# Optimization experiments

Measured on AMD Instinct MI355X. Metric: run time of the kernel, lower is better.

The kernel has to match this reference:

```python
import jax, jax.numpy as jnp
import numpy as np

BLOCK_SIZE = 64
NEG_INF = -10000.0


def setup_inputs() -> dict:
    key = jax.random.key(0)
    k1, k2, k3 = jax.random.split(key, 3)
    bs, h, s, d = 4, 12, 4096, 64
    Q = jax.random.normal(k1, (bs, h, s, d), dtype=jnp.float32)
    K = jax.random.normal(k2, (bs, h, s, d), dtype=jnp.float32)
    V = jax.random.normal(k3, (bs, h, s, d), dtype=jnp.float32)
    mask = jnp.ones((bs, s), dtype=jnp.float32)
    return {"Q": Q, "K": K, "V": V, "mask": mask}


def reference(Q, K, V, mask):
    bs, h, orig_len, d = Q.shape
    bsz = BLOCK_SIZE
    num_block = (orig_len + bsz - 1) // bsz
    pad_len = num_block * bsz - orig_len
    if pad_len > 0:
        pad4 = ((0, 0), (0, 0), (0, pad_len), (0, 0))
        Q = jnp.pad(Q, pad4)
        K = jnp.pad(K, pad4)
        V = jnp.pad(V, pad4)
        mask = jnp.pad(mask, ((0, 0), (0, pad_len)))
    # reshape into non-overlapping blocks: [bs, h, nb, bsz, d]
    Qb = Q.reshape(bs, h, num_block, bsz, d)
    Kb = K.reshape(bs, h, num_block, bsz, d)
    Vb = V.reshape(bs, h, num_block, bsz, d)
    # block-local scores (no 1/sqrt(d) scaling in the original): [bs,h,nb,bsz,bsz]
    scores = jnp.einsum('bhnxd,bhnyd->bhnxy', Qb, Kb)
    # key-side additive mask per block: -10000 where mask == 0
    remove = (mask == 0.0).reshape(bs, 1, num_block, 1, bsz)  # on key axis y
    scores = scores + jnp.where(remove, jnp.float32(NEG_INF), jnp.float32(0.0))
    probs = jax.nn.softmax(scores, axis=-1)
    # zero out rows whose query position is masked
    q_removed = (mask == 0.0).reshape(bs, 1, num_block, bsz, 1)
    probs = jnp.where(q_removed, jnp.float32(0.0), probs)
    out = jnp.einsum('bhnxy,bhnyd->bhnxd', probs, Vb)
    out = out.reshape(bs, h, num_block * bsz, d)[:, :, :orig_len, :]
    return out
```

## Files before the change

kernel.cpp:

```cpp
#include <hip/hip_runtime.h>


typedef __attribute__((ext_vector_type(8))) short bf16x8;
typedef __attribute__((ext_vector_type(4))) float f32x4;
typedef __attribute__((ext_vector_type(4))) unsigned short us4;

#define MFMA16(a, b, c) __builtin_amdgcn_mfma_f32_16x16x32_bf16((a), (b), (c), 0, 0, 0)
#define SWZ(byteoff, row) ((byteoff) ^ (((row) & 7) << 4))

static __device__ __forceinline__ unsigned short f2bf(float x) {
    union { float f; unsigned int u; } v; v.f = x;
    unsigned int r = v.u + 0x7fffu + ((v.u >> 16) & 1u);
    return (unsigned short)(r >> 16);
}
static __device__ __forceinline__ float bf2f(unsigned short b) {
    union { float f; unsigned int u; } v; v.u = ((unsigned int)b) << 16;
    return v.f;
}

__global__ __launch_bounds__(256) void lsa_kernel(
    const float* __restrict__ Q, const float* __restrict__ K,
    const float* __restrict__ V, const float* __restrict__ M,
    float* __restrict__ O)
{
    __shared__ unsigned short Kh[4096];
    __shared__ unsigned short Kl[4096];
    __shared__ unsigned short VT[4096];
    __shared__ float maskv[64];

    const int tid = threadIdx.x;
    const int gid = blockIdx.x;
    const size_t base = (size_t)gid * 4096;

    const int lane = tid & 63;
    const int wv   = tid >> 6;
    const int cc   = lane & 15;
    const int gg   = lane >> 4;
    const int qrow = wv * 16 + cc;

    const float4* Kg = (const float4*)(K + base);
    const float4* Vg = (const float4*)(V + base);
    float4 kv[4], vv[4];
#pragma unroll
    for (int it = 0; it < 4; ++it) {
        int i = tid + it * 256;
        kv[it] = Kg[i];
        vv[it] = Vg[i];
    }
    bf16x8 qfh[2], qfl[2];
#pragma unroll
    for (int s = 0; s < 2; ++s) {
        const float* qp = Q + base + (size_t)qrow * 64 + s * 32 + gg * 8;
        float4 f0 = *(const float4*)qp;
        float4 f1 = *(const float4*)(qp + 4);
        float f[8] = {f0.x, f0.y, f0.z, f0.w, f1.x, f1.y, f1.z, f1.w};
        bf16x8 h, l;
#pragma unroll
        for (int j = 0; j < 8; ++j) {
            unsigned short hb = f2bf(f[j]);
            h[j] = (short)hb;
            l[j] = (short)f2bf(f[j] - bf2f(hb));
        }
        qfh[s] = h; qfl[s] = l;
    }
    if (tid < 64) {
        int b = gid / 768;
        int blk = gid & 63;
        maskv[tid] = M[(size_t)b * 4096 + blk * 64 + tid];
    }

#pragma unroll
    for (int it = 0; it < 4; ++it) {
        int i = tid + it * 256;
        int row = i >> 4;
        int cb  = (i & 15) * 8;
        {
            float4 x = kv[it];
            us4 h, l;
            unsigned short hb;
            hb = f2bf(x.x); h.x = hb; l.x = f2bf(x.x - bf2f(hb));
            hb = f2bf(x.y); h.y = hb; l.y = f2bf(x.y - bf2f(hb));
            hb = f2bf(x.z); h.z = hb; l.z = f2bf(x.z - bf2f(hb));
            hb = f2bf(x.w); h.w = hb; l.w = f2bf(x.w - bf2f(hb));
            int by = SWZ(row * 128 + cb, row);
            *(us4*)((char*)Kh + by) = h;
            *(us4*)((char*)Kl + by) = l;
        }
        {
            float4 x = vv[it];
            int key = row, dbase = (i & 15) * 4;
            float xs[4] = {x.x, x.y, x.z, x.w};
#pragma unroll
            for (int dj = 0; dj < 4; ++dj) {
                int d = dbase + dj;
                *(unsigned short*)((char*)VT + SWZ(d * 128 + key * 2, d)) = f2bf(xs[dj]);
            }
        }
    }
    __syncthreads();

    float sc[16];
#pragma unroll
    for (int kt = 0; kt < 4; ++kt) {
        f32x4 acc = {0.f, 0.f, 0.f, 0.f};
        int krow = kt * 16 + cc;
#pragma unroll
        for (int s = 0; s < 2; ++s) {
            int by = SWZ(krow * 128 + s * 64 + gg * 16, krow);
            bf16x8 ah = *(bf16x8*)((char*)Kh + by);
            bf16x8 al = *(bf16x8*)((char*)Kl + by);
            acc = MFMA16(ah, qfh[s], acc);
            acc = MFMA16(ah, qfl[s], acc);
            acc = MFMA16(al, qfh[s], acc);
        }
#pragma unroll
        for (int r = 0; r < 4; ++r) sc[kt * 4 + r] = acc[r];
    }

    float mx = -3.0e38f;
#pragma unroll
    for (int kt = 0; kt < 4; ++kt)
#pragma unroll
        for (int r = 0; r < 4; ++r) {
            int key = kt * 16 + gg * 4 + r;
            float sv = sc[kt * 4 + r] + (maskv[key] == 0.f ? -10000.f : 0.f);
            sc[kt * 4 + r] = sv;
            mx = fmaxf(mx, sv);
        }
    mx = fmaxf(mx, __shfl_xor(mx, 16));
    mx = fmaxf(mx, __shfl_xor(mx, 32));
    float sum = 0.f;
#pragma unroll
    for (int i = 0; i < 16; ++i) { sc[i] = __expf(sc[i] - mx); sum += sc[i]; }
    sum += __shfl_xor(sum, 16);
    sum += __shfl_xor(sum, 32);
    float inv = (maskv[qrow] == 0.f ? 0.f : 1.f) / sum;

    unsigned int pku[8];
#pragma unroll
    for (int kt = 0; kt < 4; ++kt) {
        unsigned int e0 = f2bf(sc[kt * 4 + 0] * inv);
        unsigned int e1 = f2bf(sc[kt * 4 + 1] * inv);
        unsigned int e2 = f2bf(sc[kt * 4 + 2] * inv);
        unsigned int e3 = f2bf(sc[kt * 4 + 3] * inv);
        pku[kt * 2 + 0] = e0 | (e1 << 16);
        pku[kt * 2 + 1] = e2 | (e3 << 16);
    }
    const int src0 = ((2 * gg) & 3) * 16 + cc;
    const int src1 = ((2 * gg + 1) & 3) * 16 + cc;
    const bool sel = (gg >> 1) & 1;
    bf16x8 pf[2];
#pragma unroll
    for (int s = 0; s < 2; ++s) {
        unsigned int a0 = (unsigned)__shfl((int)pku[4 * s + 0], src0);
        unsigned int a1 = (unsigned)__shfl((int)pku[4 * s + 1], src0);
        unsigned int b0 = (unsigned)__shfl((int)pku[4 * s + 2], src0);
        unsigned int b1 = (unsigned)__shfl((int)pku[4 * s + 3], src0);
        unsigned int c0 = (unsigned)__shfl((int)pku[4 * s + 0], src1);
        unsigned int c1 = (unsigned)__shfl((int)pku[4 * s + 1], src1);
        unsigned int d0 = (unsigned)__shfl((int)pku[4 * s + 2], src1);
        unsigned int d1 = (unsigned)__shfl((int)pku[4 * s + 3], src1);
        union { unsigned int w[4]; bf16x8 v; } u;
        u.w[0] = sel ? b0 : a0;
        u.w[1] = sel ? b1 : a1;
        u.w[2] = sel ? d0 : c0;
        u.w[3] = sel ? d1 : c1;
        pf[s] = u.v;
    }

    float* Ob = O + base;
#pragma unroll
    for (int dt = 0; dt < 4; ++dt) {
        f32x4 o = {0.f, 0.f, 0.f, 0.f};
#pragma unroll
        for (int s = 0; s < 2; ++s) {
            int vr = dt * 16 + cc;
            bf16x8 vb = *(bf16x8*)((char*)VT + SWZ(vr * 128 + s * 64 + gg * 16, vr));
            o = MFMA16(pf[s], vb, o);
        }
#pragma unroll
        for (int r = 0; r < 4; ++r) {
            int q = wv * 16 + gg * 4 + r;
            Ob[q * 64 + dt * 16 + cc] = o[r];
        }
    }
}

extern "C" void kernel_launch(void* const* d_in, const int* in_sizes, int n_in,
                              void* d_out, int out_size, void* d_ws, size_t ws_size,
                              hipStream_t stream) {
    const float* Q = (const float*)d_in[0];
    const float* K = (const float*)d_in[1];
    const float* V = (const float*)d_in[2];
    const float* M = (const float*)d_in[3];
    float* O = (float*)d_out;
    int grid = in_sizes[0] / 4096;
    lsa_kernel<<<grid, 256, 0, stream>>>(Q, K, V, M, O);
}
```

Baseline: 36.65 us.

## Process four blocks per workgroup with double-buffered register prefetch and LDS staging

Each workgroup now handles four consecutive 64-token blocks instead of one. Global loads for the next block are issued into registers while the current block computes, and LDS is double-buffered so one barrier per block is enough. The goal is to hide global load latency behind MFMA and softmax work. The cost is a quarter as many workgroups, more register pressure and twice the LDS per workgroup, which can lower occupancy. The grid size assumes the block count is divisible by four.

New measurement: 36.32 us. No clear change (-0.9%).

```diff
diff --git a/kernel.cpp b/kernel.cpp
--- a/kernel.cpp
+++ b/kernel.cpp
@@ -23,165 +23,192 @@
     const float* __restrict__ V, const float* __restrict__ M,
     float* __restrict__ O)
 {
-    __shared__ unsigned short Kh[4096];
-    __shared__ unsigned short Kl[4096];
-    __shared__ unsigned short VT[4096];
-    __shared__ float maskv[64];
-
-    const int tid = threadIdx.x;
-    const int gid = blockIdx.x;
-    const size_t base = (size_t)gid * 4096;
-
+    __shared__ unsigned short Kh[2][4096];
+    __shared__ unsigned short Kl[2][4096];
+    __shared__ unsigned short VT[2][4096];
+    __shared__ float maskv[2][64];
+
+    const int tid  = threadIdx.x;
     const int lane = tid & 63;
     const int wv   = tid >> 6;
     const int cc   = lane & 15;
     const int gg   = lane >> 4;
     const int qrow = wv * 16 + cc;
 
-    const float4* Kg = (const float4*)(K + base);
-    const float4* Vg = (const float4*)(V + base);
-    float4 kv[4], vv[4];
-#pragma unroll
-    for (int it = 0; it < 4; ++it) {
-        int i = tid + it * 256;
-        kv[it] = Kg[i];
-        vv[it] = Vg[i];
-    }
+    const int blk0 = blockIdx.x * 4;
+
+    float4 kv[4], vv[4], qv[4];
+    float  mreg;
     bf16x8 qfh[2], qfl[2];
-#pragma unroll
-    for (int s = 0; s < 2; ++s) {
-        const float* qp = Q + base + (size_t)qrow * 64 + s * 32 + gg * 8;
-        float4 f0 = *(const float4*)qp;
-        float4 f1 = *(const float4*)(qp + 4);
-        float f[8] = {f0.x, f0.y, f0.z, f0.w, f1.x, f1.y, f1.z, f1.w};
-        bf16x8 h, l;
-#pragma unroll
-        for (int j = 0; j < 8; ++j) {
-            unsigned short hb = f2bf(f[j]);
-            h[j] = (short)hb;
-            l[j] = (short)f2bf(f[j] - bf2f(hb));
-        }
-        qfh[s] = h; qfl[s] = l;
-    }
-    if (tid < 64) {
-        int b = gid / 768;
-        int blk = gid & 63;
-        maskv[tid] = M[(size_t)b * 4096 + blk * 64 + tid];
-    }
-
-#pragma unroll
-    for (int it = 0; it < 4; ++it) {
-        int i = tid + it * 256;
-        int row = i >> 4;
-        int cb  = (i & 15) * 8;
-        {
-            float4 x = kv[it];
-            us4 h, l;
-            unsigned short hb;
-            hb = f2bf(x.x); h.x = hb; l.x = f2bf(x.x - bf2f(hb));
-            hb = f2bf(x.y); h.y = hb; l.y = f2bf(x.y - bf2f(hb));
-            hb = f2bf(x.z); h.z = hb; l.z = f2bf(x.z - bf2f(hb));
-            hb = f2bf(x.w); h.w = hb; l.w = f2bf(x.w - bf2f(hb));
-            int by = SWZ(row * 128 + cb, row);
-            *(us4*)((char*)Kh + by) = h;
-            *(us4*)((char*)Kl + by) = l;
-        }
-        {
-            float4 x = vv[it];
-            int key = row, dbase = (i & 15) * 4;
-            float xs[4] = {x.x, x.y, x.z, x.w};
-#pragma unroll
-            for (int dj = 0; dj < 4; ++dj) {
-                int d = dbase + dj;
-                *(unsigned short*)((char*)VT + SWZ(d * 128 + key * 2, d)) = f2bf(xs[dj]);
-            }
-        }
-    }
+
+    auto issue = [&](int blkid) {
+        const size_t base = (size_t)blkid * 4096;
+        const float4* Kg = (const float4*)(K + base);
+        const float4* Vg = (const float4*)(V + base);
+#pragma unroll
+        for (int it = 0; it < 4; ++it) {
+            kv[it] = Kg[tid + it * 256];
+            vv[it] = Vg[tid + it * 256];
+        }
+        const float* qb = Q + base + (size_t)qrow * 64;
+        qv[0] = *(const float4*)(qb + gg * 8);
+        qv[1] = *(const float4*)(qb + gg * 8 + 4);
+        qv[2] = *(const float4*)(qb + 32 + gg * 8);
+        qv[3] = *(const float4*)(qb + 32 + gg * 8 + 4);
+        int b  = blkid / 768;
+        int bi = blkid & 63;
+        mreg = M[(size_t)b * 4096 + bi * 64 + lane];
+    };
+
+    auto stageKV = [&](int buf) {
+#pragma unroll
+        for (int it = 0; it < 4; ++it) {
+            int i   = tid + it * 256;
+            int row = i >> 4;
+            int cb  = (i & 15) * 8;
+            {
+                float4 x = kv[it];
+                us4 h, l;
+                unsigned short hb;
+                hb = f2bf(x.x); h.x = hb; l.x = f2bf(x.x - bf2f(hb));
+                hb = f2bf(x.y); h.y = hb; l.y = f2bf(x.y - bf2f(hb));
+                hb = f2bf(x.z); h.z = hb; l.z = f2bf(x.z - bf2f(hb));
+                hb = f2bf(x.w); h.w = hb; l.w = f2bf(x.w - bf2f(hb));
+                int by = SWZ(row * 128 + cb, row);
+                *(us4*)((char*)&Kh[buf][0] + by) = h;
+                *(us4*)((char*)&Kl[buf][0] + by) = l;
+            }
+            {
+                float4 x = vv[it];
+                int key = row, dbase = (i & 15) * 4;
+                float xs[4] = {x.x, x.y, x.z, x.w};
+#pragma unroll
+                for (int dj = 0; dj < 4; ++dj) {
+                    int d = dbase + dj;
+                    *(unsigned short*)((char*)&VT[buf][0] + SWZ(d * 128 + key * 2, d)) = f2bf(xs[dj]);
+                }
+            }
+        }
+        if (tid < 64) maskv[buf][tid] = mreg;
+    };
+
+    auto stageQ = [&]() {
+#pragma unroll
+        for (int s = 0; s < 2; ++s) {
+            float4 f0 = qv[2 * s], f1 = qv[2 * s + 1];
+            float f[8] = {f0.x, f0.y, f0.z, f0.w, f1.x, f1.y, f1.z, f1.w};
+            bf16x8 h, l;
+#pragma unroll
+            for (int j = 0; j < 8; ++j) {
+                unsigned short hb = f2bf(f[j]);
+                h[j] = (short)hb;
+                l[j] = (short)f2bf(f[j] - bf2f(hb));
+            }
+            qfh[s] = h; qfl[s] = l;
+        }
+    };
+
+    auto compute = [&](int buf, int blkid) {
+        float sc[16];
+#pragma unroll
+        for (int kt = 0; kt < 4; ++kt) {
+            f32x4 acc = {0.f, 0.f, 0.f, 0.f};
+            int krow = kt * 16 + cc;
+#pragma unroll
+            for (int s = 0; s < 2; ++s) {
+                int by = SWZ(krow * 128 + s * 64 + gg * 16, krow);
+                bf16x8 ah = *(bf16x8*)((char*)&Kh[buf][0] + by);
+                bf16x8 al = *(bf16x8*)((char*)&Kl[buf][0] + by);
+                acc = MFMA16(ah, qfh[s], acc);
+                acc = MFMA16(ah, qfl[s], acc);
+                acc = MFMA16(al, qfh[s], acc);
+            }
+#pragma unroll
+            for (int r = 0; r < 4; ++r) sc[kt * 4 + r] = acc[r];
+        }
+        float mx = -3.0e38f;
+#pragma unroll
+        for (int kt = 0; kt < 4; ++kt)
+#pragma unroll
+            for (int r = 0; r < 4; ++r) {
+                int key = kt * 16 + gg * 4 + r;
+                float sv = sc[kt * 4 + r] + (maskv[buf][key] == 0.f ? -10000.f : 0.f);
+                sc[kt * 4 + r] = sv;
+                mx = fmaxf(mx, sv);
+            }
+        mx = fmaxf(mx, __shfl_xor(mx, 16));
+        mx = fmaxf(mx, __shfl_xor(mx, 32));
+        float sum = 0.f;
+#pragma unroll
+        for (int i = 0; i < 16; ++i) { sc[i] = __expf(sc[i] - mx); sum += sc[i]; }
+        sum += __shfl_xor(sum, 16);
+        sum += __shfl_xor(sum, 32);
+        float inv = (maskv[buf][qrow] == 0.f ? 0.f : 1.f) / sum;
+
+        unsigned int pku[8];
+#pragma unroll
+        for (int kt = 0; kt < 4; ++kt) {
+            unsigned int e0 = f2bf(sc[kt * 4 + 0] * inv);
+            unsigned int e1 = f2bf(sc[kt * 4 + 1] * inv);
+            unsigned int e2 = f2bf(sc[kt * 4 + 2] * inv);
+            unsigned int e3 = f2bf(sc[kt * 4 + 3] * inv);
+            pku[kt * 2 + 0] = e0 | (e1 << 16);
+            pku[kt * 2 + 1] = e2 | (e3 << 16);
+        }
+        const int src0 = ((2 * gg) & 3) * 16 + cc;
+        const int src1 = ((2 * gg + 1) & 3) * 16 + cc;
+        const bool sel = (gg >> 1) & 1;
+        bf16x8 pf[2];
+#pragma unroll
+        for (int s = 0; s < 2; ++s) {
+            unsigned int a0 = (unsigned)__shfl((int)pku[4 * s + 0], src0);
+            unsigned int a1 = (unsigned)__shfl((int)pku[4 * s + 1], src0);
+            unsigned int b0 = (unsigned)__shfl((int)pku[4 * s + 2], src0);
+            unsigned int b1 = (unsigned)__shfl((int)pku[4 * s + 3], src0);
+            unsigned int c0 = (unsigned)__shfl((int)pku[4 * s + 0], src1);
+            unsigned int c1 = (unsigned)__shfl((int)pku[4 * s + 1], src1);
+            unsigned int d0 = (unsigned)__shfl((int)pku[4 * s + 2], src1);
+            unsigned int d1 = (unsigned)__shfl((int)pku[4 * s + 3], src1);
+            union { unsigned int w[4]; bf16x8 v; } u;
+            u.w[0] = sel ? b0 : a0;
+            u.w[1] = sel ? b1 : a1;
+            u.w[2] = sel ? d0 : c0;
+            u.w[3] = sel ? d1 : c1;
+            pf[s] = u.v;
+        }
+
+        float* Ob = O + (size_t)blkid * 4096;
+#pragma unroll
+        for (int dt = 0; dt < 4; ++dt) {
+            f32x4 o = {0.f, 0.f, 0.f, 0.f};
+#pragma unroll
+            for (int s = 0; s < 2; ++s) {
+                int vr = dt * 16 + cc;
+                bf16x8 vb = *(bf16x8*)((char*)&VT[buf][0] + SWZ(vr * 128 + s * 64 + gg * 16, vr));
+                o = MFMA16(pf[s], vb, o);
+            }
+#pragma unroll
+            for (int r = 0; r < 4; ++r) {
+                int q = wv * 16 + gg * 4 + r;
+                Ob[q * 64 + dt * 16 + cc] = o[r];
+            }
+        }
+    };
+
+    issue(blk0);
+    stageKV(0);
+    stageQ();
     __syncthreads();
-
-    float sc[16];
-#pragma unroll
-    for (int kt = 0; kt < 4; ++kt) {
-        f32x4 acc = {0.f, 0.f, 0.f, 0.f};
-        int krow = kt * 16 + cc;
-#pragma unroll
-        for (int s = 0; s < 2; ++s) {
-            int by = SWZ(krow * 128 + s * 64 + gg * 16, krow);
-            bf16x8 ah = *(bf16x8*)((char*)Kh + by);
-            bf16x8 al = *(bf16x8*)((char*)Kl + by);
-            acc = MFMA16(ah, qfh[s], acc);
-            acc = MFMA16(ah, qfl[s], acc);
-            acc = MFMA16(al, qfh[s], acc);
-        }
-#pragma unroll
-        for (int r = 0; r < 4; ++r) sc[kt * 4 + r] = acc[r];
-    }
-
-    float mx = -3.0e38f;
-#pragma unroll
-    for (int kt = 0; kt < 4; ++kt)
-#pragma unroll
-        for (int r = 0; r < 4; ++r) {
-            int key = kt * 16 + gg * 4 + r;
-            float sv = sc[kt * 4 + r] + (maskv[key] == 0.f ? -10000.f : 0.f);
-            sc[kt * 4 + r] = sv;
-            mx = fmaxf(mx, sv);
-        }
-    mx = fmaxf(mx, __shfl_xor(mx, 16));
-    mx = fmaxf(mx, __shfl_xor(mx, 32));
-    float sum = 0.f;
-#pragma unroll
-    for (int i = 0; i < 16; ++i) { sc[i] = __expf(sc[i] - mx); sum += sc[i]; }
-    sum += __shfl_xor(sum, 16);
-    sum += __shfl_xor(sum, 32);
-    float inv = (maskv[qrow] == 0.f ? 0.f : 1.f) / sum;
-
-    unsigned int pku[8];
-#pragma unroll
-    for (int kt = 0; kt < 4; ++kt) {
-        unsigned int e0 = f2bf(sc[kt * 4 + 0] * inv);
-        unsigned int e1 = f2bf(sc[kt * 4 + 1] * inv);
-        unsigned int e2 = f2bf(sc[kt * 4 + 2] * inv);
-        unsigned int e3 = f2bf(sc[kt * 4 + 3] * inv);
-        pku[kt * 2 + 0] = e0 | (e1 << 16);
-        pku[kt * 2 + 1] = e2 | (e3 << 16);
-    }
-    const int src0 = ((2 * gg) & 3) * 16 + cc;
-    const int src1 = ((2 * gg + 1) & 3) * 16 + cc;
-    const bool sel = (gg >> 1) & 1;
-    bf16x8 pf[2];
-#pragma unroll
-    for (int s = 0; s < 2; ++s) {
-        unsigned int a0 = (unsigned)__shfl((int)pku[4 * s + 0], src0);
-        unsigned int a1 = (unsigned)__shfl((int)pku[4 * s + 1], src0);
-        unsigned int b0 = (unsigned)__shfl((int)pku[4 * s + 2], src0);
-        unsigned int b1 = (unsigned)__shfl((int)pku[4 * s + 3], src0);
-        unsigned int c0 = (unsigned)__shfl((int)pku[4 * s + 0], src1);
-        unsigned int c1 = (unsigned)__shfl((int)pku[4 * s + 1], src1);
-        unsigned int d0 = (unsigned)__shfl((int)pku[4 * s + 2], src1);
-        unsigned int d1 = (unsigned)__shfl((int)pku[4 * s + 3], src1);
-        union { unsigned int w[4]; bf16x8 v; } u;
-        u.w[0] = sel ? b0 : a0;
-        u.w[1] = sel ? b1 : a1;
-        u.w[2] = sel ? d0 : c0;
-        u.w[3] = sel ? d1 : c1;
-        pf[s] = u.v;
-    }
-
-    float* Ob = O + base;
-#pragma unroll
-    for (int dt = 0; dt < 4; ++dt) {
-        f32x4 o = {0.f, 0.f, 0.f, 0.f};
-#pragma unroll
-        for (int s = 0; s < 2; ++s) {
-            int vr = dt * 16 + cc;
-            bf16x8 vb = *(bf16x8*)((char*)VT + SWZ(vr * 128 + s * 64 + gg * 16, vr));
-            o = MFMA16(pf[s], vb, o);
-        }
-#pragma unroll
-        for (int r = 0; r < 4; ++r) {
-            int q = wv * 16 + gg * 4 + r;
-            Ob[q * 64 + dt * 16 + cc] = o[r];
+    issue(blk0 + 1);
+#pragma unroll
+    for (int i = 0; i < 4; ++i) {
+        const int cur = i & 1;
+        compute(cur, blk0 + i);
+        if (i < 3) {
+            stageKV(1 - cur);
+            stageQ();
+            __syncthreads();
+            if (i < 2) issue(blk0 + i + 2);
         }
     }
 }
@@ -194,6 +221,7 @@
     const float* V = (const float*)d_in[2];
     const float* M = (const float*)d_in[3];
     float* O = (float*)d_out;
-    int grid = in_sizes[0] / 4096;
+    int nblk = in_sizes[0] / 4096;
+    int grid = nblk / 4;
     lsa_kernel<<<grid, 256, 0, stream>>>(Q, K, V, M, O);
 }
```

## Load V fragments directly from global memory instead of transposing through LDS

Applied to the files above, without the earlier changes.

Removes the shared-memory transposed V buffer and its scalar scattered writes. Each lane now reads its MFMA B-operand V elements straight from global memory with strided scalar loads, software-prefetching the next d-tile while computing the current one. This cuts LDS footprint and LDS write traffic but replaces coalesced float4 loads with 64-element-strided scalar loads, each wave re-reading all of V for its tile.

After: 35.85 us, median of 2. 2.2% less time.

```diff
diff --git a/kernel.cpp b/kernel.cpp
--- a/kernel.cpp
+++ b/kernel.cpp
@@ -25,11 +25,10 @@
 {
     __shared__ unsigned short Kh[4096];
     __shared__ unsigned short Kl[4096];
-    __shared__ unsigned short VT[4096];
     __shared__ float maskv[64];
 
-    const int tid = threadIdx.x;
-    const int gid = blockIdx.x;
+    const int tid  = threadIdx.x;
+    const int gid  = blockIdx.x;
     const size_t base = (size_t)gid * 4096;
 
     const int lane = tid & 63;
@@ -39,14 +38,10 @@
     const int qrow = wv * 16 + cc;
 
     const float4* Kg = (const float4*)(K + base);
-    const float4* Vg = (const float4*)(V + base);
-    float4 kv[4], vv[4];
-#pragma unroll
-    for (int it = 0; it < 4; ++it) {
-        int i = tid + it * 256;
-        kv[it] = Kg[i];
-        vv[it] = Vg[i];
-    }
+    float4 kv[4];
+#pragma unroll
+    for (int it = 0; it < 4; ++it) kv[it] = Kg[tid + it * 256];
+
     bf16x8 qfh[2], qfl[2];
 #pragma unroll
     for (int s = 0; s < 2; ++s) {
@@ -71,31 +66,19 @@
 
 #pragma unroll
     for (int it = 0; it < 4; ++it) {
-        int i = tid + it * 256;
+        int i   = tid + it * 256;
         int row = i >> 4;
         int cb  = (i & 15) * 8;
-        {
-            float4 x = kv[it];
-            us4 h, l;
-            unsigned short hb;
-            hb = f2bf(x.x); h.x = hb; l.x = f2bf(x.x - bf2f(hb));
-            hb = f2bf(x.y); h.y = hb; l.y = f2bf(x.y - bf2f(hb));
-            hb = f2bf(x.z); h.z = hb; l.z = f2bf(x.z - bf2f(hb));
-            hb = f2bf(x.w); h.w = hb; l.w = f2bf(x.w - bf2f(hb));
-            int by = SWZ(row * 128 + cb, row);
-            *(us4*)((char*)Kh + by) = h;
-            *(us4*)((char*)Kl + by) = l;
-        }
-        {
-            float4 x = vv[it];
-            int key = row, dbase = (i & 15) * 4;
-            float xs[4] = {x.x, x.y, x.z, x.w};
-#pragma unroll
-            for (int dj = 0; dj < 4; ++dj) {
-                int d = dbase + dj;
-                *(unsigned short*)((char*)VT + SWZ(d * 128 + key * 2, d)) = f2bf(xs[dj]);
-            }
-        }
+        float4 x = kv[it];
+        us4 h, l;
+        unsigned short hb;
+        hb = f2bf(x.x); h.x = hb; l.x = f2bf(x.x - bf2f(hb));
+        hb = f2bf(x.y); h.y = hb; l.y = f2bf(x.y - bf2f(hb));
+        hb = f2bf(x.z); h.z = hb; l.z = f2bf(x.z - bf2f(hb));
+        hb = f2bf(x.w); h.w = hb; l.w = f2bf(x.w - bf2f(hb));
+        int by = SWZ(row * 128 + cb, row);
+        *(us4*)((char*)Kh + by) = h;
+        *(us4*)((char*)Kl + by) = l;
     }
     __syncthreads();
 
@@ -115,6 +98,15 @@
         }
 #pragma unroll
         for (int r = 0; r < 4; ++r) sc[kt * 4 + r] = acc[r];
+    }
+
+    const float* Vb = V + base;
+    float vf[16], vn[16];
+    {
+        const float* p0 = Vb + (size_t)(0 * 32 + gg * 8) * 64 + 0 * 16 + cc;
+        const float* p1 = Vb + (size_t)(1 * 32 + gg * 8) * 64 + 0 * 16 + cc;
+#pragma unroll
+        for (int j = 0; j < 8; ++j) { vf[j] = p0[j * 64]; vf[8 + j] = p1[j * 64]; }
     }
 
     float mx = -3.0e38f;
@@ -171,18 +163,28 @@
     float* Ob = O + base;
 #pragma unroll
     for (int dt = 0; dt < 4; ++dt) {
+        if (dt < 3) {
+            const float* p0 = Vb + (size_t)(0 * 32 + gg * 8) * 64 + (dt + 1) * 16 + cc;
+            const float* p1 = Vb + (size_t)(1 * 32 + gg * 8) * 64 + (dt + 1) * 16 + cc;
+#pragma unroll
+            for (int j = 0; j < 8; ++j) { vn[j] = p0[j * 64]; vn[8 + j] = p1[j * 64]; }
+        }
+        bf16x8 vb0, vb1;
+#pragma unroll
+        for (int j = 0; j < 8; ++j) {
+            vb0[j] = (short)f2bf(vf[j]);
+            vb1[j] = (short)f2bf(vf[8 + j]);
+        }
         f32x4 o = {0.f, 0.f, 0.f, 0.f};
-#pragma unroll
-        for (int s = 0; s < 2; ++s) {
-            int vr = dt * 16 + cc;
-            bf16x8 vb = *(bf16x8*)((char*)VT + SWZ(vr * 128 + s * 64 + gg * 16, vr));
-            o = MFMA16(pf[s], vb, o);
-        }
+        o = MFMA16(pf[0], vb0, o);
+        o = MFMA16(pf[1], vb1, o);
 #pragma unroll
         for (int r = 0; r < 4; ++r) {
             int q = wv * 16 + gg * 4 + r;
             Ob[q * 64 + dt * 16 + cc] = o[r];
         }
+#pragma unroll
+        for (int j = 0; j < 16; ++j) vf[j] = vn[j];
     }
 }
 
```
